# Kernel tuning notes

Measured on AMD Instinct MI355X. Metric: run time of the kernel, lower is better.

Reference implementation:

```python
import jax, jax.numpy as jnp
import numpy as np


def _chamfer_min_sqdist(a, b):
    # a: [N,3], b: [M,3] -> for each point in a, min squared distance to b. [N]
    # ||a||^2 + ||b||^2 - 2 a.b^T ; clamp tiny negatives from cancellation.
    a2 = jnp.sum(a * a, axis=-1)            # [N]
    b2 = jnp.sum(b * b, axis=-1)            # [M]
    cross = a @ b.T                          # [N,M] GEMM, K=3
    d = a2[:, None] + b2[None, :] - 2.0 * cross
    return jnp.maximum(jnp.min(d, axis=1), 0.0)


def setup_inputs() -> dict:
    key = jax.random.key(0)
    k1, k2 = jax.random.split(key)
    N = 16384
    state_x = jax.random.normal(k1, (N, 3), dtype=jnp.float32)
    target = jax.random.normal(k2, (N, 3), dtype=jnp.float32)
    return {"state_x": state_x, "target": target}


def reference(state_x, target):
    # dist1: target -> nearest in state_x ; dist2: state_x -> nearest in target
    dist1 = _chamfer_min_sqdist(target, state_x)   # [N]
    dist2 = _chamfer_min_sqdist(state_x, target)   # [N]
    loss = (jnp.mean(jnp.sqrt(dist1)) + jnp.mean(jnp.sqrt(dist2))) * 0.5
    return loss * 10.0
```

## Files before the change

kernel.cpp:

```cpp
#include <hip/hip_runtime.h>
#include <math.h>


typedef float v2f __attribute__((ext_vector_type(2)));

#define QPT 16
#define TILE_PAIRS 64

__device__ __forceinline__ unsigned enc_f32(float f) {
    int b = __float_as_int(f);
    return (b >= 0) ? ((unsigned)b | 0x80000000u) : ~(unsigned)b;
}
__device__ __forceinline__ float dec_f32(unsigned k) {
    int b = (k & 0x80000000u) ? (int)(k & 0x7FFFFFFFu) : ~(int)k;
    return __int_as_float(b);
}

__global__ __launch_bounds__(256) void chamfer_partial_min(
    const float* __restrict__ state_x, const float* __restrict__ target,
    unsigned* __restrict__ mins_u, int N, int S)
{
    const int tid = threadIdx.x;
    const int qchunk = blockIdx.x / S;
    const int s = blockIdx.x % S;
    const int qbase = qchunk * (256 * QPT);

    const float* qcloud;
    const float* db;
    int qoff;
    if (qbase < N) { qcloud = target;  db = state_x; qoff = qbase;     }
    else           { qcloud = state_x; db = target;  qoff = qbase - N; }

    v2f mx[QPT], my[QPT], mz[QPT];
    float m[QPT];
    #pragma unroll
    for (int q = 0; q < QPT; ++q) {
        const int qidx = qoff + q * 256 + tid;
        const float x = -2.0f * qcloud[3 * qidx + 0];
        const float y = -2.0f * qcloud[3 * qidx + 1];
        const float z = -2.0f * qcloud[3 * qidx + 2];
        mx[q] = (v2f){x, x};
        my[q] = (v2f){y, y};
        mz[q] = (v2f){z, z};
        m[q] = 3.0e38f;
    }

    __shared__ float4 tile[TILE_PAIRS * 2];

    const int sliceN = N / S;
    const int base0 = s * sliceN;

    for (int t0 = 0; t0 < sliceN; t0 += 2 * TILE_PAIRS) {
        if (tid < TILE_PAIRS) {
            const int g0 = base0 + t0 + 2 * tid;
            const float x0 = db[3 * g0 + 0], y0 = db[3 * g0 + 1], z0 = db[3 * g0 + 2];
            const float x1 = db[3 * g0 + 3], y1 = db[3 * g0 + 4], z1 = db[3 * g0 + 5];
            tile[2 * tid + 0] = make_float4(x0, x1, y0, y1);
            tile[2 * tid + 1] = make_float4(z0, z1,
                                            fmaf(x0, x0, fmaf(y0, y0, z0 * z0)),
                                            fmaf(x1, x1, fmaf(y1, y1, z1 * z1)));
        }
        __syncthreads();

        #pragma unroll 2
        for (int p = 0; p < TILE_PAIRS; ++p) {
            const float4 A = tile[2 * p + 0];
            const float4 B = tile[2 * p + 1];
            const v2f X = (v2f){A.x, A.y};
            const v2f Y = (v2f){A.z, A.w};
            const v2f Z = (v2f){B.x, B.y};
            const v2f W = (v2f){B.z, B.w};
            #pragma unroll
            for (int q = 0; q < QPT; ++q) {
                v2f d = __builtin_elementwise_fma(X, mx[q], W);
                d = __builtin_elementwise_fma(Y, my[q], d);
                d = __builtin_elementwise_fma(Z, mz[q], d);
                m[q] = fminf(fminf(m[q], d.x), d.y);
            }
        }
        __syncthreads();
    }

    #pragma unroll
    for (int q = 0; q < QPT; ++q) {
        const int qi = qbase + q * 256 + tid;
        atomicMin(&mins_u[qi], enc_f32(m[q]));
    }
}

__global__ __launch_bounds__(256) void chamfer_finish(
    const float* __restrict__ state_x, const float* __restrict__ target,
    const unsigned* __restrict__ mins_u, float* __restrict__ out, int N)
{
    const int tid = threadIdx.x;
    const int qi = blockIdx.x * 256 + tid;

    const float* qcloud = (qi < N) ? target : state_x;
    const int qidx = (qi < N) ? qi : qi - N;
    const float qx = qcloud[3 * qidx + 0];
    const float qy = qcloud[3 * qidx + 1];
    const float qz = qcloud[3 * qidx + 2];
    const float a2 = qx * qx + qy * qy + qz * qz;

    const float mm = dec_f32(mins_u[qi]);
    float v = sqrtf(fmaxf(a2 + mm, 0.0f));

    for (int off = 32; off > 0; off >>= 1) v += __shfl_down(v, off, 64);
    __shared__ float wsum[4];
    if ((tid & 63) == 0) wsum[tid >> 6] = v;
    __syncthreads();
    if (tid == 0) {
        const float bsum = wsum[0] + wsum[1] + wsum[2] + wsum[3];
        atomicAdd(out, bsum * 5.0f / (float)N);
    }
}

extern "C" void kernel_launch(void* const* d_in, const int* in_sizes, int n_in,
                              void* d_out, int out_size, void* d_ws, size_t ws_size,
                              hipStream_t stream)
{
    const float* state_x = (const float*)d_in[0];
    const float* target  = (const float*)d_in[1];
    float* out = (float*)d_out;

    const int N = in_sizes[0] / 3;
    const int twoN = 2 * N;
    const int nQChunks = twoN / (256 * QPT);

    int S = 128;
    while (S > 1 && (N / S) % (2 * TILE_PAIRS) != 0) S >>= 1;

    unsigned* mins_u = (unsigned*)d_ws;

    hipMemsetAsync(mins_u, 0xFF, (size_t)twoN * sizeof(unsigned), stream);
    hipMemsetAsync(d_out, 0, sizeof(float), stream);
    chamfer_partial_min<<<nQChunks * S, 256, 0, stream>>>(state_x, target, mins_u, N, S);
    chamfer_finish<<<twoN / 256, 256, 0, stream>>>(state_x, target, mins_u, out, N);
}
```

Before: 99.79 us.

## Precompute packed point pairs and stream them via uniform global loads instead of LDS

```diff
diff --git a/kernel.cpp b/kernel.cpp
--- a/kernel.cpp
+++ b/kernel.cpp
@@ -4,8 +4,9 @@
 
 typedef float v2f __attribute__((ext_vector_type(2)));
 
-#define QPT 16
-#define TILE_PAIRS 64
+#define QPT 8
+
+struct Pair { float4 a; float4 b; };
 
 __device__ __forceinline__ unsigned enc_f32(float f) {
     int b = __float_as_int(f);
@@ -16,20 +17,44 @@
     return __int_as_float(b);
 }
 
-__global__ __launch_bounds__(256) void chamfer_partial_min(
+__global__ __launch_bounds__(256) void chamfer_prep(
     const float* __restrict__ state_x, const float* __restrict__ target,
-    unsigned* __restrict__ mins_u, int N, int S)
+    Pair* __restrict__ pairs, unsigned* __restrict__ mins_u,
+    float* __restrict__ out, int N)
+{
+    const int t = blockIdx.x * 256 + threadIdx.x;
+    const int half = N >> 1;
+    const float* src = (t < half) ? state_x : target;
+    const int j = 2 * ((t < half) ? t : t - half);
+    const float x0 = src[3*j+0], y0 = src[3*j+1], z0 = src[3*j+2];
+    const float x1 = src[3*j+3], y1 = src[3*j+4], z1 = src[3*j+5];
+    Pair p;
+    p.a = make_float4(x0, x1, y0, y1);
+    p.b = make_float4(z0, z1,
+                      fmaf(x0, x0, fmaf(y0, y0, z0 * z0)),
+                      fmaf(x1, x1, fmaf(y1, y1, z1 * z1)));
+    pairs[t] = p;
+    mins_u[2*t+0] = 0xFFFFFFFFu;
+    mins_u[2*t+1] = 0xFFFFFFFFu;
+    if (t == 0) *out = 0.0f;
+}
+
+__global__ __launch_bounds__(256) void chamfer_main(
+    const float* __restrict__ state_x, const float* __restrict__ target,
+    const Pair* __restrict__ pairs, unsigned* __restrict__ mins_u,
+    int N, int S)
 {
     const int tid = threadIdx.x;
     const int qchunk = blockIdx.x / S;
     const int s = blockIdx.x % S;
     const int qbase = qchunk * (256 * QPT);
+    const int half = N >> 1;
 
     const float* qcloud;
-    const float* db;
+    const Pair* db;
     int qoff;
-    if (qbase < N) { qcloud = target;  db = state_x; qoff = qbase;     }
-    else           { qcloud = state_x; db = target;  qoff = qbase - N; }
+    if (qbase < N) { qcloud = target;  db = pairs;        qoff = qbase;     }
+    else           { qcloud = state_x; db = pairs + half; qoff = qbase - N; }
 
     v2f mx[QPT], my[QPT], mz[QPT];
     float m[QPT];
@@ -45,40 +70,24 @@
         m[q] = 3.0e38f;
     }
 
-    __shared__ float4 tile[TILE_PAIRS * 2];
+    const int pps = half / S;
+    const Pair* pk = db + s * pps;
 
-    const int sliceN = N / S;
-    const int base0 = s * sliceN;
-
-    for (int t0 = 0; t0 < sliceN; t0 += 2 * TILE_PAIRS) {
-        if (tid < TILE_PAIRS) {
-            const int g0 = base0 + t0 + 2 * tid;
-            const float x0 = db[3 * g0 + 0], y0 = db[3 * g0 + 1], z0 = db[3 * g0 + 2];
-            const float x1 = db[3 * g0 + 3], y1 = db[3 * g0 + 4], z1 = db[3 * g0 + 5];
-            tile[2 * tid + 0] = make_float4(x0, x1, y0, y1);
-            tile[2 * tid + 1] = make_float4(z0, z1,
-                                            fmaf(x0, x0, fmaf(y0, y0, z0 * z0)),
-                                            fmaf(x1, x1, fmaf(y1, y1, z1 * z1)));
+    #pragma unroll 4
+    for (int p = 0; p < pps; ++p) {
+        const float4 A = pk[p].a;
+        const float4 B = pk[p].b;
+        const v2f X = (v2f){A.x, A.y};
+        const v2f Y = (v2f){A.z, A.w};
+        const v2f Z = (v2f){B.x, B.y};
+        const v2f W = (v2f){B.z, B.w};
+        #pragma unroll
+        for (int q = 0; q < QPT; ++q) {
+            v2f d = __builtin_elementwise_fma(X, mx[q], W);
+            d = __builtin_elementwise_fma(Y, my[q], d);
+            d = __builtin_elementwise_fma(Z, mz[q], d);
+            m[q] = fminf(fminf(m[q], d.x), d.y);
         }
-        __syncthreads();
-
-        #pragma unroll 2
-        for (int p = 0; p < TILE_PAIRS; ++p) {
-            const float4 A = tile[2 * p + 0];
-            const float4 B = tile[2 * p + 1];
-            const v2f X = (v2f){A.x, A.y};
-            const v2f Y = (v2f){A.z, A.w};
-            const v2f Z = (v2f){B.x, B.y};
-            const v2f W = (v2f){B.z, B.w};
-            #pragma unroll
-            for (int q = 0; q < QPT; ++q) {
-                v2f d = __builtin_elementwise_fma(X, mx[q], W);
-                d = __builtin_elementwise_fma(Y, my[q], d);
-                d = __builtin_elementwise_fma(Z, mz[q], d);
-                m[q] = fminf(fminf(m[q], d.x), d.y);
-            }
-        }
-        __syncthreads();
     }
 
     #pragma unroll
@@ -125,15 +134,16 @@
 
     const int N = in_sizes[0] / 3;
     const int twoN = 2 * N;
+
+    int S = 64;
+    while (S > 1 && ((N / 2) % S) != 0) S >>= 1;
+
+    unsigned* mins_u = (unsigned*)d_ws;
+    Pair* pairs = (Pair*)((char*)d_ws + (size_t)twoN * sizeof(unsigned));
+
     const int nQChunks = twoN / (256 * QPT);
 
-    int S = 128;
-    while (S > 1 && (N / S) % (2 * TILE_PAIRS) != 0) S >>= 1;
-
-    unsigned* mins_u = (unsigned*)d_ws;
-
-    hipMemsetAsync(mins_u, 0xFF, (size_t)twoN * sizeof(unsigned), stream);
-    hipMemsetAsync(d_out, 0, sizeof(float), stream);
-    chamfer_partial_min<<<nQChunks * S, 256, 0, stream>>>(state_x, target, mins_u, N, S);
+    chamfer_prep<<<N / 256, 256, 0, stream>>>(state_x, target, pairs, mins_u, out, N);
+    chamfer_main<<<nQChunks * S, 256, 0, stream>>>(state_x, target, pairs, mins_u, N, S);
     chamfer_finish<<<twoN / 256, 256, 0, stream>>>(state_x, target, mins_u, out, N);
 }
```

New measurement: 95.52 us. 4.3% less time.

## Compute chamfer distances with bf16 split-precision MFMA instead of packed FP32 FMAs

Applied to the files above, without the earlier changes.

```diff
diff --git a/kernel.cpp b/kernel.cpp
--- a/kernel.cpp
+++ b/kernel.cpp
@@ -2,10 +2,10 @@
 #include <math.h>
 
 
-typedef float v2f __attribute__((ext_vector_type(2)));
+typedef __attribute__((ext_vector_type(8)))  short bf16x8;
+typedef __attribute__((ext_vector_type(16))) float f32x16;
 
-#define QPT 16
-#define TILE_PAIRS 64
+#define S_SLICES 8
 
 __device__ __forceinline__ unsigned enc_f32(float f) {
     int b = __float_as_int(f);
@@ -16,94 +16,129 @@
     return __int_as_float(b);
 }
 
-__global__ __launch_bounds__(256) void chamfer_partial_min(
+__device__ __forceinline__ unsigned short f2bf(float v) {
+    unsigned u = __float_as_uint(v);
+    u += 0x7FFFu + ((u >> 16) & 1u);
+    return (unsigned short)(u >> 16);
+}
+__device__ __forceinline__ float bf2f(unsigned short b) {
+    unsigned u = ((unsigned)b) << 16;
+    return __uint_as_float(u);
+}
+__device__ __forceinline__ unsigned pk2(unsigned short lo, unsigned short hi) {
+    return (unsigned)lo | ((unsigned)hi << 16);
+}
+
+__global__ __launch_bounds__(256) void chamfer_prep(
     const float* __restrict__ state_x, const float* __restrict__ target,
+    uint4* __restrict__ AfragS, uint4* __restrict__ AfragT,
+    uint4* __restrict__ BfragS, uint4* __restrict__ BfragT,
+    unsigned* __restrict__ mins_u, float* __restrict__ out, int N)
+{
+    const int p = blockIdx.x * 256 + threadIdx.x;
+    const float* src = (p < N) ? state_x : target;
+    const int i = (p < N) ? p : p - N;
+
+    const float x = src[3*i+0], y = src[3*i+1], z = src[3*i+2];
+    const float n2 = fmaf(x, x, fmaf(y, y, z * z));
+
+    const unsigned short hx = f2bf(x), hy = f2bf(y), hz = f2bf(z);
+    const unsigned short lx = f2bf(x - bf2f(hx));
+    const unsigned short ly = f2bf(y - bf2f(hy));
+    const unsigned short lz = f2bf(z - bf2f(hz));
+    const unsigned short mhx = f2bf(-2.0f*x), mhy = f2bf(-2.0f*y), mhz = f2bf(-2.0f*z);
+    const unsigned short mlx = f2bf(-2.0f*x - bf2f(mhx));
+    const unsigned short mly = f2bf(-2.0f*y - bf2f(mhy));
+    const unsigned short mlz = f2bf(-2.0f*z - bf2f(mhz));
+    const unsigned short hn = f2bf(n2);
+    const unsigned short ln = f2bf(n2 - bf2f(hn));
+    const unsigned short ONE = 0x3F80;
+
+    uint4 A0 = make_uint4(pk2(mhx,mhy), pk2(mhz,mlx), pk2(mly,mlz), pk2(mhx,mhy));
+    uint4 A1 = make_uint4(pk2(mhz,mlx), pk2(mly,mlz), pk2(hn,ln),   pk2(ONE,ONE));
+    uint4 B0 = make_uint4(pk2(hx,hy), pk2(hz,hx), pk2(hy,hz), pk2(lx,ly));
+    uint4 B1 = make_uint4(pk2(lz,lx), pk2(ly,lz), pk2(ONE,ONE), pk2(hn,ln));
+
+    uint4* Aarr = (p < N) ? AfragS : AfragT;
+    uint4* Barr = (p < N) ? BfragS : BfragT;
+    Aarr[2*i+0] = A0;  Aarr[2*i+1] = A1;
+    Barr[2*i+0] = B0;  Barr[2*i+1] = B1;
+
+    mins_u[p] = 0xFFFFFFFFu;
+    if (p == 0) *out = 0.0f;
+}
+
+__global__ __launch_bounds__(256) void chamfer_main(
+    const bf16x8* __restrict__ AfragS, const bf16x8* __restrict__ AfragT,
+    const bf16x8* __restrict__ BfragS, const bf16x8* __restrict__ BfragT,
     unsigned* __restrict__ mins_u, int N, int S)
 {
-    const int tid = threadIdx.x;
-    const int qchunk = blockIdx.x / S;
-    const int s = blockIdx.x % S;
-    const int qbase = qchunk * (256 * QPT);
+    const int tid  = threadIdx.x;
+    const int lane = tid & 63;
+    const int l31  = lane & 31;
+    const int half = lane >> 5;
+    const int w    = tid >> 6;
 
-    const float* qcloud;
-    const float* db;
-    int qoff;
-    if (qbase < N) { qcloud = target;  db = state_x; qoff = qbase;     }
-    else           { qcloud = state_x; db = target;  qoff = qbase - N; }
+    const int bs = blockIdx.x / S;
+    const int s  = blockIdx.x % S;
+    const int qrow0 = bs * 128 + w * 32;
 
-    v2f mx[QPT], my[QPT], mz[QPT];
-    float m[QPT];
+    const bf16x8* afr;
+    const bf16x8* bfr;
+    if (qrow0 < N) { afr = AfragT + (size_t)qrow0 * 2;       bfr = BfragS; }
+    else           { afr = AfragS + (size_t)(qrow0 - N) * 2; bfr = BfragT; }
+
+    const bf16x8 av = afr[l31 * 2 + half];
+
+    const int C = N / S;
+    const bf16x8* bp = bfr + (size_t)(s * C) * 2;
+    const int boff = l31 * 2 + half;
+
+    f32x16 racc;
     #pragma unroll
-    for (int q = 0; q < QPT; ++q) {
-        const int qidx = qoff + q * 256 + tid;
-        const float x = -2.0f * qcloud[3 * qidx + 0];
-        const float y = -2.0f * qcloud[3 * qidx + 1];
-        const float z = -2.0f * qcloud[3 * qidx + 2];
-        mx[q] = (v2f){x, x};
-        my[q] = (v2f){y, y};
-        mz[q] = (v2f){z, z};
-        m[q] = 3.0e38f;
-    }
+    for (int i = 0; i < 16; ++i) racc[i] = 3.0e38f;
+    f32x16 zc;
+    #pragma unroll
+    for (int i = 0; i < 16; ++i) zc[i] = 0.0f;
 
-    __shared__ float4 tile[TILE_PAIRS * 2];
-
-    const int sliceN = N / S;
-    const int base0 = s * sliceN;
-
-    for (int t0 = 0; t0 < sliceN; t0 += 2 * TILE_PAIRS) {
-        if (tid < TILE_PAIRS) {
-            const int g0 = base0 + t0 + 2 * tid;
-            const float x0 = db[3 * g0 + 0], y0 = db[3 * g0 + 1], z0 = db[3 * g0 + 2];
-            const float x1 = db[3 * g0 + 3], y1 = db[3 * g0 + 4], z1 = db[3 * g0 + 5];
-            tile[2 * tid + 0] = make_float4(x0, x1, y0, y1);
-            tile[2 * tid + 1] = make_float4(z0, z1,
-                                            fmaf(x0, x0, fmaf(y0, y0, z0 * z0)),
-                                            fmaf(x1, x1, fmaf(y1, y1, z1 * z1)));
-        }
-        __syncthreads();
-
-        #pragma unroll 2
-        for (int p = 0; p < TILE_PAIRS; ++p) {
-            const float4 A = tile[2 * p + 0];
-            const float4 B = tile[2 * p + 1];
-            const v2f X = (v2f){A.x, A.y};
-            const v2f Y = (v2f){A.z, A.w};
-            const v2f Z = (v2f){B.x, B.y};
-            const v2f W = (v2f){B.z, B.w};
-            #pragma unroll
-            for (int q = 0; q < QPT; ++q) {
-                v2f d = __builtin_elementwise_fma(X, mx[q], W);
-                d = __builtin_elementwise_fma(Y, my[q], d);
-                d = __builtin_elementwise_fma(Z, mz[q], d);
-                m[q] = fminf(fminf(m[q], d.x), d.y);
-            }
-        }
-        __syncthreads();
+    #pragma unroll 2
+    for (int it = 0; it < C / 64; ++it) {
+        const bf16x8 b0 = bp[it * 128 + boff];
+        const bf16x8 b1 = bp[it * 128 + 64 + boff];
+        f32x16 acc0 = __builtin_amdgcn_mfma_f32_32x32x16_bf16(av, b0, zc, 0, 0, 0);
+        f32x16 acc1 = __builtin_amdgcn_mfma_f32_32x32x16_bf16(av, b1, zc, 0, 0, 0);
+        #pragma unroll
+        for (int i = 0; i < 16; ++i)
+            racc[i] = fminf(fminf(racc[i], acc0[i]), acc1[i]);
     }
 
     #pragma unroll
-    for (int q = 0; q < QPT; ++q) {
-        const int qi = qbase + q * 256 + tid;
-        atomicMin(&mins_u[qi], enc_f32(m[q]));
+    for (int i = 0; i < 16; ++i) {
+        float v = racc[i];
+        v = fminf(v, __shfl_xor(v, 16, 64));
+        v = fminf(v, __shfl_xor(v,  8, 64));
+        v = fminf(v, __shfl_xor(v,  4, 64));
+        v = fminf(v, __shfl_xor(v,  2, 64));
+        v = fminf(v, __shfl_xor(v,  1, 64));
+        racc[i] = v;
+    }
+
+    if (l31 == 0) {
+        #pragma unroll
+        for (int i = 0; i < 16; ++i) {
+            const int row = (i & 3) + 8 * (i >> 2) + 4 * half;
+            atomicMin(&mins_u[qrow0 + row], enc_f32(racc[i]));
+        }
     }
 }
 
 __global__ __launch_bounds__(256) void chamfer_finish(
-    const float* __restrict__ state_x, const float* __restrict__ target,
     const unsigned* __restrict__ mins_u, float* __restrict__ out, int N)
 {
     const int tid = threadIdx.x;
     const int qi = blockIdx.x * 256 + tid;
 
-    const float* qcloud = (qi < N) ? target : state_x;
-    const int qidx = (qi < N) ? qi : qi - N;
-    const float qx = qcloud[3 * qidx + 0];
-    const float qy = qcloud[3 * qidx + 1];
-    const float qz = qcloud[3 * qidx + 2];
-    const float a2 = qx * qx + qy * qy + qz * qz;
-
-    const float mm = dec_f32(mins_u[qi]);
-    float v = sqrtf(fmaxf(a2 + mm, 0.0f));
+    float v = sqrtf(fmaxf(dec_f32(mins_u[qi]), 0.0f));
 
     for (int off = 32; off > 0; off >>= 1) v += __shfl_down(v, off, 64);
     __shared__ float wsum[4];
@@ -125,15 +160,24 @@
 
     const int N = in_sizes[0] / 3;
     const int twoN = 2 * N;
-    const int nQChunks = twoN / (256 * QPT);
 
-    int S = 128;
-    while (S > 1 && (N / S) % (2 * TILE_PAIRS) != 0) S >>= 1;
+    int S = S_SLICES;
+    while (S > 1 && (N % (S * 64)) != 0) S >>= 1;
 
-    unsigned* mins_u = (unsigned*)d_ws;
+    char* wsb = (char*)d_ws;
+    unsigned* mins_u = (unsigned*)wsb;
+    uint4* AfragS = (uint4*)(wsb + (size_t)twoN * 4);
+    uint4* AfragT = (uint4*)(wsb + (size_t)twoN * 4 + (size_t)N * 32);
+    uint4* BfragS = (uint4*)(wsb + (size_t)twoN * 4 + (size_t)N * 64);
+    uint4* BfragT = (uint4*)(wsb + (size_t)twoN * 4 + (size_t)N * 96);
 
-    hipMemsetAsync(mins_u, 0xFF, (size_t)twoN * sizeof(unsigned), stream);
-    hipMemsetAsync(d_out, 0, sizeof(float), stream);
-    chamfer_partial_min<<<nQChunks * S, 256, 0, stream>>>(state_x, target, mins_u, N, S);
-    chamfer_finish<<<twoN / 256, 256, 0, stream>>>(state_x, target, mins_u, out, N);
+    chamfer_prep<<<twoN / 256, 256, 0, stream>>>(
+        state_x, target, AfragS, AfragT, BfragS, BfragT, mins_u, out, N);
+
+    const int rowBlocks = twoN / 128;
+    chamfer_main<<<rowBlocks * S, 256, 0, stream>>>(
+        (const bf16x8*)AfragS, (const bf16x8*)AfragT,
+        (const bf16x8*)BfragS, (const bf16x8*)BfragT, mins_u, N, S);
+
+    chamfer_finish<<<twoN / 256, 256, 0, stream>>>(mins_u, out, N);
 }
```

Measured after the change: 91.36 us. 8.4% less time.
